# Optimization experiments

Measured on AMD Instinct MI355X. Metric: run time of the kernel, lower is better.

The kernel has to match this reference:

```python
import jax, jax.numpy as jnp
import numpy as np

NUM_HEADS = 32
NUM_KV_HEADS = 8
HEAD_DIM = 128
HIDDEN = 4096
ROPE_THETA = 10000.0
SLIDING_WINDOW = 1024
NEG_INF = -1e9


def _make_sliding_window_mask(q_len, kv_len, window):
    # additive mask: 0 where attendable (causal AND within window), -inf otherwise
    i = jnp.arange(q_len)[:, None]
    j = jnp.arange(kv_len)[None, :]
    allowed = (j <= i) & (j > i - window)
    return jnp.where(allowed, 0.0, NEG_INF).astype(jnp.float32)[None, None]  # [1,1,q,kv]


def _rope_tables(seq_len, head_dim, theta):
    inv_freq = 1.0 / (theta ** (jnp.arange(0, head_dim, 2, dtype=jnp.float32) / head_dim))
    t = jnp.arange(seq_len, dtype=jnp.float32)
    freqs = jnp.einsum('i,j->ij', t, inv_freq)        # [S, D/2]
    emb = jnp.concatenate([freqs, freqs], axis=-1)     # [S, D]
    return jnp.cos(emb), jnp.sin(emb)


def _rotate_half(x):
    d = x.shape[-1] // 2
    return jnp.concatenate([-x[..., d:], x[..., :d]], axis=-1)


def setup_inputs() -> dict:
    key = jax.random.key(0)
    ks = jax.random.split(key, 5)
    B, S = 1, 2048
    sc = 0.02
    hidden_states = jax.random.normal(ks[0], (B, S, HIDDEN), dtype=jnp.float32)
    Wq = jax.random.normal(ks[1], (HIDDEN, NUM_HEADS * HEAD_DIM), dtype=jnp.float32) * sc
    Wk = jax.random.normal(ks[2], (HIDDEN, NUM_KV_HEADS * HEAD_DIM), dtype=jnp.float32) * sc
    Wv = jax.random.normal(ks[3], (HIDDEN, NUM_KV_HEADS * HEAD_DIM), dtype=jnp.float32) * sc
    Wo = jax.random.normal(ks[4], (NUM_HEADS * HEAD_DIM, HIDDEN), dtype=jnp.float32) * sc
    attention_mask = _make_sliding_window_mask(S, S, SLIDING_WINDOW)
    position_ids = jnp.arange(S, dtype=jnp.int64)[None, :]
    return {"hidden_states": hidden_states, "attention_mask": attention_mask,
            "position_ids": position_ids, "Wq": Wq, "Wk": Wk, "Wv": Wv, "Wo": Wo}


def reference(hidden_states, attention_mask, position_ids, Wq, Wk, Wv, Wo):
    B, S, _ = hidden_states.shape
    # projections
    q = (hidden_states @ Wq).reshape(B, S, NUM_HEADS, HEAD_DIM).transpose(0, 2, 1, 3)      # [B,H,S,D]
    k = (hidden_states @ Wk).reshape(B, S, NUM_KV_HEADS, HEAD_DIM).transpose(0, 2, 1, 3)   # [B,Hk,S,D]
    v = (hidden_states @ Wv).reshape(B, S, NUM_KV_HEADS, HEAD_DIM).transpose(0, 2, 1, 3)
    # RoPE
    cos_t, sin_t = _rope_tables(S, HEAD_DIM, ROPE_THETA)
    cos = cos_t[position_ids][:, None]  # [B,1,S,D]
    sin = sin_t[position_ids][:, None]
    q = q * cos + _rotate_half(q) * sin
    k = k * cos + _rotate_half(k) * sin
    # repeat_kv (GQA): [B,Hk,S,D] -> [B,H,S,D]
    n_rep = NUM_HEADS // NUM_KV_HEADS
    k = jnp.repeat(k, n_rep, axis=1)
    v = jnp.repeat(v, n_rep, axis=1)
    # attention
    scores = jnp.einsum('bhqd,bhkd->bhqk', q, k) / np.sqrt(HEAD_DIM)
    scores = scores + attention_mask
    probs = jax.nn.softmax(scores, axis=-1)
    out = jnp.einsum('bhqk,bhkd->bhqd', probs, v)
    out = out.transpose(0, 2, 1, 3).reshape(B, S, HIDDEN)
    return out @ Wo
```

## Files before the change

kernel.cpp:

```cpp
#include <hip/hip_runtime.h>

typedef __attribute__((ext_vector_type(8))) short short8;
typedef __attribute__((ext_vector_type(4))) short s16x4;
typedef __attribute__((ext_vector_type(4))) float f32x4;
typedef unsigned short u16;
typedef unsigned int u32;

__device__ __forceinline__ u16 f2bf(float f) {
  union { float f; unsigned int u; } v; v.f = f;
  unsigned int r = (v.u + 0x7FFFu + ((v.u >> 16) & 1u)) >> 16;
  return (u16)r;
}
__device__ __forceinline__ float bf2f(u16 b) {
  union { unsigned int u; float f; } v; v.u = ((unsigned int)b) << 16;
  return v.f;
}
__device__ __forceinline__ void load_lds16(const void* g, void* l) {
  __builtin_amdgcn_global_load_lds((const __attribute__((address_space(1))) void*)g,
                                   (__attribute__((address_space(3))) void*)l, 16, 0, 0);
}

__global__ void cvt_f32_bf16_kernel(const float* __restrict__ in, u16* __restrict__ out, int n4) {
  int i = blockIdx.x * blockDim.x + threadIdx.x;
  if (i >= n4) return;
  float4 v = ((const float4*)in)[i];
  ushort4 o;
  o.x = f2bf(v.x); o.y = f2bf(v.y); o.z = f2bf(v.z); o.w = f2bf(v.w);
  ((ushort4*)out)[i] = o;
}

__global__ void combine_bf16_kernel(u16* __restrict__ d, const u16* __restrict__ p, int n8) {
  int i = blockIdx.x * blockDim.x + threadIdx.x;
  if (i >= n8) return;
  short8 a = ((const short8*)d)[i];
  short8 b = ((const short8*)p)[i];
  short8 o;
#pragma unroll
  for (int j = 0; j < 8; ++j) o[j] = (short)f2bf(bf2f((u16)a[j]) + bf2f((u16)b[j]));
  ((short8*)d)[i] = o;
}
__global__ void combine2_f32_kernel(float* __restrict__ out, const u16* __restrict__ p0,
                                    const u16* __restrict__ p1, int n8) {
  int i = blockIdx.x * blockDim.x + threadIdx.x;
  if (i >= n8) return;
  short8 a = ((const short8*)p0)[i];
  short8 b = ((const short8*)p1)[i];
  float4 o0, o1;
  o0.x = bf2f((u16)a[0]) + bf2f((u16)b[0]);
  o0.y = bf2f((u16)a[1]) + bf2f((u16)b[1]);
  o0.z = bf2f((u16)a[2]) + bf2f((u16)b[2]);
  o0.w = bf2f((u16)a[3]) + bf2f((u16)b[3]);
  o1.x = bf2f((u16)a[4]) + bf2f((u16)b[4]);
  o1.y = bf2f((u16)a[5]) + bf2f((u16)b[5]);
  o1.z = bf2f((u16)a[6]) + bf2f((u16)b[6]);
  o1.w = bf2f((u16)a[7]) + bf2f((u16)b[7]);
  ((float4*)out)[i * 2]     = o0;
  ((float4*)out)[i * 2 + 1] = o1;
}

__device__ __forceinline__ void tconv64_tile(const float* __restrict__ W, u16* __restrict__ Wt,
                                             int K, int N, int nb, int kb, int tid) {
  __shared__ float tile[64][65];
  int tx = tid & 15, ty = tid >> 4;
  const float* src = W + (size_t)(kb + ty) * N + nb + tx * 4;
#pragma unroll
  for (int i = 0; i < 4; ++i) {
    float4 v = *(const float4*)(src + (size_t)i * 16 * N);
    tile[ty + i * 16][tx * 4 + 0] = v.x;
    tile[ty + i * 16][tx * 4 + 1] = v.y;
    tile[ty + i * 16][tx * 4 + 2] = v.z;
    tile[ty + i * 16][tx * 4 + 3] = v.w;
  }
  __syncthreads();
  u16* dst = Wt + (size_t)(nb + ty) * K + kb + tx * 4;
#pragma unroll
  for (int i = 0; i < 4; ++i) {
    s16x4 o;
#pragma unroll
    for (int j = 0; j < 4; ++j) o[j] = (short)f2bf(tile[tx * 4 + j][ty + i * 16]);
    *(s16x4*)(dst + (size_t)i * 16 * K) = o;
  }
}

__global__ void tconv3_kernel(const float* __restrict__ Wq, const float* __restrict__ Wk,
                              const float* __restrict__ Wv, u16* __restrict__ WqT,
                              u16* __restrict__ WkvT) {
  int id = blockIdx.x;
  if (id < 4096)      tconv64_tile(Wq, WqT, 4096, 4096, (id & 63) * 64, (id >> 6) * 64, threadIdx.x);
  else if (id < 5120) { int t = id - 4096; tconv64_tile(Wk, WkvT, 4096, 1024, (t & 15) * 64, (t >> 4) * 64, threadIdx.x); }
  else                { int t = id - 5120; tconv64_tile(Wv, WkvT + (size_t)1024 * 4096, 4096, 1024, (t & 15) * 64, (t >> 4) * 64, threadIdx.x); }
}

__global__ void tconv1_kernel(const float* __restrict__ W, u16* __restrict__ Wt) {
  int id = blockIdx.x;
  tconv64_tile(W, Wt, 4096, 4096, (id & 63) * 64, (id >> 6) * 64, threadIdx.x);
}

__global__ void rope_kernel(u16* __restrict__ Qb, u16* __restrict__ Kb) {
  int idx = blockIdx.x * blockDim.x + threadIdx.x;
  u16* X; int ld, hmask, hshift, id; float scale;
  if (idx < 4194304) { X = Qb; ld = 4096; hmask = 31; hshift = 5; id = idx;           scale = 0.12751781828987514f; }
  else               { X = Kb; ld = 1024; hmask = 7;  hshift = 3; id = idx - 4194304; scale = 1.0f; }
  int j = id & 63;
  int t = id >> 6;
  int hh = t & hmask;
  int s = t >> hshift;
  float invf = exp2f(-(float)j * (13.287712379549449f / 64.0f));
  float ang = (float)s * invf;
  float sn, cs;
  sincosf(ang, &sn, &cs);
  u16* p = X + (size_t)s * ld + hh * 128 + j;
  float a = bf2f(p[0]), b = bf2f(p[64]);
  p[0]  = f2bf((a * cs - b * sn) * scale);
  p[64] = f2bf((b * cs + a * sn) * scale);
}

__global__ __launch_bounds__(256, 2) void gemm_kv_kernel(
    const u16* __restrict__ A, const u16* __restrict__ B,
    u16* __restrict__ Kb, u16* __restrict__ Vt, int N, int K) {
  __shared__ u16 As[2][128 * 64];
  __shared__ u16 Bs[2][128 * 64];
  int tid = threadIdx.x, lane = tid & 63, w = tid >> 6;
  int wr = w >> 1, wc = w & 1;
  int g = lane >> 4, q = lane & 15;
  int nbx = gridDim.x;
  int flat = blockIdx.y * nbx + blockIdx.x;
  int cpx = (nbx * gridDim.y) >> 3;
  flat = (flat & 7) * cpx + (flat >> 3);
  int m0 = (flat / nbx) * 128, n0 = (flat % nbx) * 128;
  f32x4 acc[4][4];
#pragma unroll
  for (int i = 0; i < 4; ++i)
#pragma unroll
    for (int j = 0; j < 4; ++j) acc[i][j] = (f32x4){0.f, 0.f, 0.f, 0.f};
  int srow = tid >> 3;
  int scol = ((tid & 7) ^ (srow & 7)) << 3;
  const u16* ga = A + (size_t)(m0 + srow) * K + scol;
  const u16* gb = B + (size_t)(n0 + srow) * K + scol;
  int xorm = (q & 7) << 3;
  int arow = wr * 64 + q;
  int brow = wc * 64 + q;
  int nt = K >> 6;

  auto stage = [&](int buf, int t) {
    const u16* pa = ga + t * 64;
    const u16* pb = gb + t * 64;
#pragma unroll
    for (int it = 0; it < 4; ++it) {
      load_lds16(pa + (size_t)it * 32 * K, (char*)(&As[buf][0]) + (it * 256 + w * 64) * 16);
      load_lds16(pb + (size_t)it * 32 * K, (char*)(&Bs[buf][0]) + (it * 256 + w * 64) * 16);
    }
  };

  stage(0, 0);
  stage(1, 1);
  asm volatile("s_waitcnt vmcnt(8)" ::: "memory");
  __builtin_amdgcn_s_barrier();
  for (int t = 0; t < nt; ++t) {
    int cur = t & 1;
    short8 af[2][4], bfr[2][4];
#pragma unroll
    for (int kb = 0; kb < 2; ++kb) {
      int col = (kb * 32 + g * 8) ^ xorm;
#pragma unroll
      for (int m = 0; m < 4; ++m) af[kb][m]  = *(const short8*)&As[cur][(arow + m * 16) * 64 + col];
#pragma unroll
      for (int n = 0; n < 4; ++n) bfr[kb][n] = *(const short8*)&Bs[cur][(brow + n * 16) * 64 + col];
    }
    asm volatile("s_waitcnt lgkmcnt(0)" ::: "memory");
    __builtin_amdgcn_s_barrier();
    if (t + 2 < nt) stage(cur, t + 2);
    __builtin_amdgcn_sched_barrier(0);
    __builtin_amdgcn_s_setprio(1);
#pragma unroll
    for (int kb = 0; kb < 2; ++kb)
#pragma unroll
      for (int m = 0; m < 4; ++m)
#pragma unroll
        for (int n = 0; n < 4; ++n)
          acc[m][n] = __builtin_amdgcn_mfma_f32_16x16x32_bf16(af[kb][m], bfr[kb][n], acc[m][n], 0, 0, 0);
    __builtin_amdgcn_s_setprio(0);
    if (t + 2 < nt)      { asm volatile("s_waitcnt vmcnt(8)" ::: "memory"); }
    else if (t + 1 < nt) { asm volatile("s_waitcnt vmcnt(0)" ::: "memory"); }
    __builtin_amdgcn_s_barrier();
  }
  int crow = m0 + wr * 64 + g * 4;
  int ccol = n0 + wc * 64 + q;
  if (n0 < 1024) {
#pragma unroll
    for (int m = 0; m < 4; ++m)
#pragma unroll
      for (int n = 0; n < 4; ++n)
#pragma unroll
        for (int r = 0; r < 4; ++r)
          Kb[(size_t)(crow + m * 16 + r) * 1024 + ccol + n * 16] = f2bf(acc[m][n][r]);
  } else {
#pragma unroll
    for (int n = 0; n < 4; ++n) {
      int vcol = ccol + n * 16 - 1024;
#pragma unroll
      for (int m = 0; m < 4; ++m) {
        s16x4 o;
#pragma unroll
        for (int r = 0; r < 4; ++r) o[r] = (short)f2bf(acc[m][n][r]);
        *(s16x4*)(Vt + (size_t)vcol * 2048 + crow + m * 16) = o;
      }
    }
  }
}

__global__ __launch_bounds__(512, 1) void gemm256_kernel(
    const u16* __restrict__ A, const u16* __restrict__ B,
    u16* __restrict__ C0, u16* __restrict__ C1, int N, int K, int KH) {
  __shared__ u16 As[2][256 * 64];
  __shared__ u16 Bs[2][256 * 64];
  int tid = threadIdx.x, lane = tid & 63, wid = tid >> 6;
  int wr = wid >> 2, wc = wid & 3;
  int g = lane >> 4, q = lane & 15;
  int id = blockIdx.z * gridDim.x * gridDim.y + blockIdx.y * gridDim.x + blockIdx.x;
  int tot = gridDim.x * gridDim.y * gridDim.z;
  int swz = (id & 7) * (tot >> 3) + (id >> 3);
  int perh = gridDim.x * gridDim.y;
  int z = swz / perh, rem = swz % perh;
  int m0 = (rem / gridDim.x) * 256, n0 = (rem % gridDim.x) * 256;
  int k0 = z * KH;
  f32x4 acc[8][4];
#pragma unroll
  for (int i = 0; i < 8; ++i)
#pragma unroll
    for (int j = 0; j < 4; ++j) acc[i][j] = (f32x4){0.f, 0.f, 0.f, 0.f};
  int srow = tid >> 3;
  int scol = ((tid & 7) ^ (srow & 7)) << 3;
  const u16* ga = A + (size_t)(m0 + srow) * K + k0 + scol;
  const u16* gb = B + (size_t)(n0 + srow) * K + k0 + scol;
  int xorm = (q & 7) << 3;
  int arow = wr * 128 + q;
  int brow = wc * 64 + q;
  int nt = KH >> 6;

  auto stage = [&](int buf, int t) {
    const u16* pa = ga + t * 64;
    const u16* pb = gb + t * 64;
#pragma unroll
    for (int it = 0; it < 4; ++it) {
      load_lds16(pa + (size_t)it * 64 * K, (char*)(&As[buf][0]) + it * 8192 + tid * 16);
      load_lds16(pb + (size_t)it * 64 * K, (char*)(&Bs[buf][0]) + it * 8192 + tid * 16);
    }
  };

  stage(0, 0);
  stage(1, 1);
  asm volatile("s_waitcnt vmcnt(8)" ::: "memory");
  __builtin_amdgcn_s_barrier();
  for (int t = 0; t < nt; ++t) {
    int cur = t & 1;
    int col0 = (g * 8) ^ xorm;
    short8 a0[8], b0[4];
#pragma unroll
    for (int m = 0; m < 8; ++m) a0[m] = *(const short8*)&As[cur][(arow + m * 16) * 64 + col0];
#pragma unroll
    for (int n = 0; n < 4; ++n) b0[n] = *(const short8*)&Bs[cur][(brow + n * 16) * 64 + col0];
    __builtin_amdgcn_s_setprio(1);
#pragma unroll
    for (int m = 0; m < 8; ++m)
#pragma unroll
      for (int n = 0; n < 4; ++n)
        acc[m][n] = __builtin_amdgcn_mfma_f32_16x16x32_bf16(a0[m], b0[n], acc[m][n], 0, 0, 0);
    __builtin_amdgcn_s_setprio(0);
    int col1 = (32 + g * 8) ^ xorm;
    short8 a1[8], b1[4];
#pragma unroll
    for (int m = 0; m < 8; ++m) a1[m] = *(const short8*)&As[cur][(arow + m * 16) * 64 + col1];
#pragma unroll
    for (int n = 0; n < 4; ++n) b1[n] = *(const short8*)&Bs[cur][(brow + n * 16) * 64 + col1];
    asm volatile("s_waitcnt lgkmcnt(0)" ::: "memory");
    __builtin_amdgcn_s_barrier();
    if (t + 2 < nt) stage(cur, t + 2);
    __builtin_amdgcn_sched_barrier(0);
    __builtin_amdgcn_s_setprio(1);
#pragma unroll
    for (int m = 0; m < 8; ++m)
#pragma unroll
      for (int n = 0; n < 4; ++n)
        acc[m][n] = __builtin_amdgcn_mfma_f32_16x16x32_bf16(a1[m], b1[n], acc[m][n], 0, 0, 0);
    __builtin_amdgcn_s_setprio(0);
    if (t + 2 < nt)      { asm volatile("s_waitcnt vmcnt(8)" ::: "memory"); }
    else if (t + 1 < nt) { asm volatile("s_waitcnt vmcnt(0)" ::: "memory"); }
    __builtin_amdgcn_s_barrier();
  }
  int crow = m0 + wr * 128 + g * 4;
  int ccol = n0 + wc * 64 + q;
  u16* dst = z ? C1 : C0;
#pragma unroll
  for (int fm = 0; fm < 8; ++fm)
#pragma unroll
    for (int fn = 0; fn < 4; ++fn)
#pragma unroll
      for (int r = 0; r < 4; ++r)
        dst[(size_t)(crow + fm * 16 + r) * N + ccol + fn * 16] = f2bf(acc[fm][fn][r]);
}

__global__ __launch_bounds__(512, 4) void attn_kernel(
    const u16* __restrict__ Q, const u16* __restrict__ Kg,
    const u16* __restrict__ Vt, u16* __restrict__ O) {
  __shared__ u16 Ks[2][64 * 128];
  __shared__ u16 Vs[2][128 * 64];
  int tid = threadIdx.x, lane = tid & 63, w = tid >> 6;
  int wg = w >> 2;
  int g = lane >> 4, q = lane & 15;
  int q0 = blockIdx.x * 128;
  int h = blockIdx.y, hk = h >> 2;
  int qbase = q0 + wg * 64;
  int qrow = qbase + (w & 3) * 16;
  int xorm = (lane & 7) << 3;
  short8 qf[4];
  {
    const u16* qp = Q + (size_t)(qrow + q) * 4096 + h * 128 + g * 8;
#pragma unroll
    for (int kk = 0; kk < 4; ++kk) qf[kk] = *(const short8*)(qp + kk * 32);
  }
  float mrow = -1e30f, lsum = 0.f;
  f32x4 of[8];
#pragma unroll
  for (int d = 0; d < 8; ++d) of[d] = (f32x4){0.f, 0.f, 0.f, 0.f};
  int bjt_lo = (q0 >= 1024) ? ((q0 - 1023) >> 6) : 0;
  int bjt_hi = (q0 + 64) >> 6;
  int wjt_lo = (qbase >= 1024) ? ((qbase - 1023) >> 6) : 0;
  int wjt_hi = qbase >> 6;
  int krow = tid >> 4;
  int kchunk = (tid & 15) ^ (krow & 7);
  const u16* kbase = Kg + (size_t)krow * 1024 + hk * 128 + (kchunk << 3);
  int vrow = tid >> 3;
  int vchunk = (tid & 7) ^ (vrow & 7);
  const u16* vbase = Vt + (size_t)(hk * 128 + vrow) * 2048 + (vchunk << 3);

  auto stageK = [&](int buf, int j0) {
    const u16* gp = kbase + (size_t)j0 * 1024;
#pragma unroll
    for (int it = 0; it < 2; ++it)
      load_lds16(gp + (size_t)it * 32 * 1024, (char*)(&Ks[buf][0]) + it * 8192 + tid * 16);
  };
  auto stageV = [&](int buf, int j0) {
    const u16* gp = vbase + j0;
#pragma unroll
    for (int it = 0; it < 2; ++it)
      load_lds16(gp + (size_t)it * 64 * 2048, (char*)(&Vs[buf][0]) + it * 8192 + tid * 16);
  };

  int cur = 0;
  stageK(0, bjt_lo << 6);
  stageV(0, bjt_lo << 6);
  asm volatile("s_waitcnt vmcnt(0)" ::: "memory");
  __syncthreads();
  for (int jt = bjt_lo; jt <= bjt_hi; ++jt) {
    int j0 = jt << 6;
    if (jt < bjt_hi) { stageK(cur ^ 1, j0 + 64); stageV(cur ^ 1, j0 + 64); }
    if (jt >= wjt_lo && jt <= wjt_hi) {
      f32x4 sf[4];
#pragma unroll
      for (int nt = 0; nt < 4; ++nt) sf[nt] = (f32x4){0.f, 0.f, 0.f, 0.f};
      const u16* ks = &Ks[cur][0];
      __builtin_amdgcn_s_setprio(1);
#pragma unroll
      for (int kk = 0; kk < 4; ++kk) {
        short8 qv = qf[kk];
        int col = (kk * 32 + g * 8) ^ xorm;
#pragma unroll
        for (int nt = 0; nt < 4; ++nt) {
          short8 kf = *(const short8*)&ks[(nt * 16 + q) * 128 + col];
          sf[nt] = __builtin_amdgcn_mfma_f32_16x16x32_bf16(kf, qv, sf[nt], 0, 0, 0);
        }
      }
      __builtin_amdgcn_s_setprio(0);
      float p[4][4];
#pragma unroll
      for (int nt = 0; nt < 4; ++nt)
#pragma unroll
        for (int r = 0; r < 4; ++r) p[nt][r] = sf[nt][r];
      if (j0 + 63 > qrow || j0 + 1009 <= qrow) {
        int qq = qrow + q;
        int kb = j0 + g * 4;
#pragma unroll
        for (int nt = 0; nt < 4; ++nt)
#pragma unroll
          for (int r = 0; r < 4; ++r) {
            int key = kb + nt * 16 + r;
            if (key > qq || key + 1024 <= qq) p[nt][r] = -1e9f;
          }
      }
      float tm = p[0][0];
#pragma unroll
      for (int nt = 0; nt < 4; ++nt)
#pragma unroll
        for (int r = 0; r < 4; ++r) tm = fmaxf(tm, p[nt][r]);
      tm = fmaxf(tm, __shfl_xor(tm, 16));
      tm = fmaxf(tm, __shfl_xor(tm, 32));
      if (__any(tm > mrow + 8.f)) {
        float nm = fmaxf(mrow, tm);
        float sc = __builtin_amdgcn_exp2f(mrow - nm);
        mrow = nm;
        lsum *= sc;
#pragma unroll
        for (int d = 0; d < 8; ++d) of[d] *= sc;
      }
      float ps = 0.f;
#pragma unroll
      for (int nt = 0; nt < 4; ++nt)
#pragma unroll
        for (int r = 0; r < 4; ++r) {
          float e = __builtin_amdgcn_exp2f(p[nt][r] - mrow);
          p[nt][r] = e;
          ps += e;
        }
      ps += __shfl_xor(ps, 16);
      ps += __shfl_xor(ps, 32);
      lsum += ps;
      u32 pk[4][2];
#pragma unroll
      for (int nt = 0; nt < 4; ++nt) {
        pk[nt][0] = __builtin_amdgcn_perm(__float_as_uint(p[nt][1]), __float_as_uint(p[nt][0]), 0x07060302u);
        pk[nt][1] = __builtin_amdgcn_perm(__float_as_uint(p[nt][3]), __float_as_uint(p[nt][2]), 0x07060302u);
      }
      int s0 = q + ((g & 1) ? 32 : 0);
      int s1 = s0 + 16;
      bool hi_sel = g >= 2;
      const u16* vs = &Vs[cur][0];
      __builtin_amdgcn_s_setprio(1);
#pragma unroll
      for (int kh = 0; kh < 2; ++kh) {
        int lo = kh * 2, hi = lo + 1;
        u32 a0 = (u32)__shfl((int)pk[lo][0], s0);
        u32 a1 = (u32)__shfl((int)pk[lo][1], s0);
        u32 b0 = (u32)__shfl((int)pk[hi][0], s0);
        u32 b1 = (u32)__shfl((int)pk[hi][1], s0);
        u32 a2 = (u32)__shfl((int)pk[lo][0], s1);
        u32 a3 = (u32)__shfl((int)pk[lo][1], s1);
        u32 b2 = (u32)__shfl((int)pk[hi][0], s1);
        u32 b3 = (u32)__shfl((int)pk[hi][1], s1);
        union { u32 u[4]; short8 s; } pb;
        pb.u[0] = hi_sel ? b0 : a0;
        pb.u[1] = hi_sel ? b1 : a1;
        pb.u[2] = hi_sel ? b2 : a2;
        pb.u[3] = hi_sel ? b3 : a3;
        int col = (kh * 32 + g * 8) ^ xorm;
#pragma unroll
        for (int dt = 0; dt < 8; ++dt) {
          short8 vv = *(const short8*)&vs[(dt * 16 + q) * 64 + col];
          of[dt] = __builtin_amdgcn_mfma_f32_16x16x32_bf16(vv, pb.s, of[dt], 0, 0, 0);
        }
      }
      __builtin_amdgcn_s_setprio(0);
    }
    asm volatile("s_waitcnt vmcnt(0)" ::: "memory");
    __builtin_amdgcn_s_barrier();
    cur ^= 1;
  }
  float inv = 1.f / lsum;
  u16* op = O + (size_t)(qrow + q) * 4096 + h * 128 + g * 4;
#pragma unroll
  for (int dt = 0; dt < 8; ++dt) {
    s16x4 o4;
#pragma unroll
    for (int r = 0; r < 4; ++r) o4[r] = (short)f2bf(of[dt][r] * inv);
    *(s16x4*)(op + dt * 16) = o4;
  }
}

extern "C" void kernel_launch(void* const* d_in, const int* in_sizes, int n_in,
                              void* d_out, int out_size, void* d_ws, size_t ws_size,
                              hipStream_t stream) {
  (void)in_sizes; (void)n_in; (void)out_size;
  const float* hs = (const float*)d_in[0];
  const float* Wq = (const float*)d_in[3];
  const float* Wk = (const float*)d_in[4];
  const float* Wv = (const float*)d_in[5];
  const float* Wo = (const float*)d_in[6];
  float* out = (float*)d_out;
  char* ws = (char*)d_ws;

  u16* Xb   = (u16*)(ws + 0);
  u16* Wt   = (u16*)(ws + 16777216);
  u16* WkvT = (u16*)(ws + 50331648);
  u16* Qb   = (u16*)(ws + 67108864);
  u16* Kb   = (u16*)(ws + 83886080);
  u16* Vtb  = (u16*)(ws + 88080384);
  u16* Ab   = (u16*)(ws + 96468992);
  u16* P1q  = Ab;
  u16* P0o  = WkvT;
  u16* P1o  = Qb;
  if (ws_size < 113246208u) return;

  cvt_f32_bf16_kernel<<<dim3(2097152 / 256), 256, 0, stream>>>(hs, Xb, 2097152);

  tconv3_kernel<<<dim3(6144), 256, 0, stream>>>(Wq, Wk, Wv, Wt, WkvT);

  gemm256_kernel<<<dim3(16, 8, 2), 512, 0, stream>>>(Xb, Wt, Qb, P1q, 4096, 4096, 2048);
  combine_bf16_kernel<<<dim3(4096), 256, 0, stream>>>(Qb, P1q, 1048576);

  gemm_kv_kernel<<<dim3(16, 16), 256, 0, stream>>>(Xb, WkvT, Kb, Vtb, 2048, 4096);

  rope_kernel<<<dim3(20480), 256, 0, stream>>>(Qb, Kb);

  attn_kernel<<<dim3(16, 32), 512, 0, stream>>>(Qb, Kb, Vtb, Ab);

  tconv1_kernel<<<dim3(4096), 256, 0, stream>>>(Wo, Wt);
  gemm256_kernel<<<dim3(16, 8, 2), 512, 0, stream>>>(Ab, Wt, P0o, P1o, 4096, 4096, 2048);
  combine2_f32_kernel<<<dim3(4096), 256, 0, stream>>>(out, P0o, P1o, 1048576);
}
```

Measured before the change: 324.0 us.

## Split-K KV projection with 256 tiles and fold Q partial combine into RoPE

The KV projection GEMM moves from 128x128 tiles on 256 blocks to 256x256 tiles with a 4-way K split (256 blocks), writing bf16 partials into the freed Wt buffer. A new combine kernel sums those partials into K and transposed V. The separate Q split-K combine kernel is removed, and its addition now happens inside the RoPE kernel. This cuts one launch and one full pass over Q, and gives the KV GEMM better tile reuse, at the cost of extra partial-buffer traffic and bf16 rounding of each partial.

New measurement: 311.7 us. 3.8% less time.

```diff
diff --git a/kernel.cpp b/kernel.cpp
--- a/kernel.cpp
+++ b/kernel.cpp
@@ -29,16 +29,6 @@
   ((ushort4*)out)[i] = o;
 }
 
-__global__ void combine_bf16_kernel(u16* __restrict__ d, const u16* __restrict__ p, int n8) {
-  int i = blockIdx.x * blockDim.x + threadIdx.x;
-  if (i >= n8) return;
-  short8 a = ((const short8*)d)[i];
-  short8 b = ((const short8*)p)[i];
-  short8 o;
-#pragma unroll
-  for (int j = 0; j < 8; ++j) o[j] = (short)f2bf(bf2f((u16)a[j]) + bf2f((u16)b[j]));
-  ((short8*)d)[i] = o;
-}
 __global__ void combine2_f32_kernel(float* __restrict__ out, const u16* __restrict__ p0,
                                     const u16* __restrict__ p1, int n8) {
   int i = blockIdx.x * blockDim.x + threadIdx.x;
@@ -58,6 +48,25 @@
   ((float4*)out)[i * 2 + 1] = o1;
 }
 
+__global__ void combine_kv_kernel(const u16* __restrict__ PKV, u16* __restrict__ Kb,
+                                  u16* __restrict__ Vt) {
+  int i = blockIdx.x * blockDim.x + threadIdx.x;
+  const u16* src; u16* dst; size_t off;
+  if (i < 262144) { off = (size_t)i; dst = Kb; src = PKV; }
+  else            { off = (size_t)(i - 262144); dst = Vt; src = PKV + 2097152; }
+  float s[8] = {0.f, 0.f, 0.f, 0.f, 0.f, 0.f, 0.f, 0.f};
+#pragma unroll
+  for (int z = 0; z < 4; ++z) {
+    short8 v = *(const short8*)(src + (size_t)z * 4194304 + off * 8);
+#pragma unroll
+    for (int j = 0; j < 8; ++j) s[j] += bf2f((u16)v[j]);
+  }
+  short8 o;
+#pragma unroll
+  for (int j = 0; j < 8; ++j) o[j] = (short)f2bf(s[j]);
+  ((short8*)dst)[off] = o;
+}
+
 __device__ __forceinline__ void tconv64_tile(const float* __restrict__ W, u16* __restrict__ Wt,
                                              int K, int N, int nb, int kb, int tid) {
   __shared__ float tile[64][65];
@@ -96,116 +105,34 @@
   tconv64_tile(W, Wt, 4096, 4096, (id & 63) * 64, (id >> 6) * 64, threadIdx.x);
 }
 
-__global__ void rope_kernel(u16* __restrict__ Qb, u16* __restrict__ Kb) {
+__global__ void rope_kernel(u16* __restrict__ Qb, const u16* __restrict__ Qp1, u16* __restrict__ Kb) {
   int idx = blockIdx.x * blockDim.x + threadIdx.x;
-  u16* X; int ld, hmask, hshift, id; float scale;
-  if (idx < 4194304) { X = Qb; ld = 4096; hmask = 31; hshift = 5; id = idx;           scale = 0.12751781828987514f; }
-  else               { X = Kb; ld = 1024; hmask = 7;  hshift = 3; id = idx - 4194304; scale = 1.0f; }
-  int j = id & 63;
-  int t = id >> 6;
-  int hh = t & hmask;
-  int s = t >> hshift;
-  float invf = exp2f(-(float)j * (13.287712379549449f / 64.0f));
-  float ang = (float)s * invf;
-  float sn, cs;
-  sincosf(ang, &sn, &cs);
-  u16* p = X + (size_t)s * ld + hh * 128 + j;
-  float a = bf2f(p[0]), b = bf2f(p[64]);
-  p[0]  = f2bf((a * cs - b * sn) * scale);
-  p[64] = f2bf((b * cs + a * sn) * scale);
-}
-
-__global__ __launch_bounds__(256, 2) void gemm_kv_kernel(
-    const u16* __restrict__ A, const u16* __restrict__ B,
-    u16* __restrict__ Kb, u16* __restrict__ Vt, int N, int K) {
-  __shared__ u16 As[2][128 * 64];
-  __shared__ u16 Bs[2][128 * 64];
-  int tid = threadIdx.x, lane = tid & 63, w = tid >> 6;
-  int wr = w >> 1, wc = w & 1;
-  int g = lane >> 4, q = lane & 15;
-  int nbx = gridDim.x;
-  int flat = blockIdx.y * nbx + blockIdx.x;
-  int cpx = (nbx * gridDim.y) >> 3;
-  flat = (flat & 7) * cpx + (flat >> 3);
-  int m0 = (flat / nbx) * 128, n0 = (flat % nbx) * 128;
-  f32x4 acc[4][4];
-#pragma unroll
-  for (int i = 0; i < 4; ++i)
-#pragma unroll
-    for (int j = 0; j < 4; ++j) acc[i][j] = (f32x4){0.f, 0.f, 0.f, 0.f};
-  int srow = tid >> 3;
-  int scol = ((tid & 7) ^ (srow & 7)) << 3;
-  const u16* ga = A + (size_t)(m0 + srow) * K + scol;
-  const u16* gb = B + (size_t)(n0 + srow) * K + scol;
-  int xorm = (q & 7) << 3;
-  int arow = wr * 64 + q;
-  int brow = wc * 64 + q;
-  int nt = K >> 6;
-
-  auto stage = [&](int buf, int t) {
-    const u16* pa = ga + t * 64;
-    const u16* pb = gb + t * 64;
-#pragma unroll
-    for (int it = 0; it < 4; ++it) {
-      load_lds16(pa + (size_t)it * 32 * K, (char*)(&As[buf][0]) + (it * 256 + w * 64) * 16);
-      load_lds16(pb + (size_t)it * 32 * K, (char*)(&Bs[buf][0]) + (it * 256 + w * 64) * 16);
-    }
-  };
-
-  stage(0, 0);
-  stage(1, 1);
-  asm volatile("s_waitcnt vmcnt(8)" ::: "memory");
-  __builtin_amdgcn_s_barrier();
-  for (int t = 0; t < nt; ++t) {
-    int cur = t & 1;
-    short8 af[2][4], bfr[2][4];
-#pragma unroll
-    for (int kb = 0; kb < 2; ++kb) {
-      int col = (kb * 32 + g * 8) ^ xorm;
-#pragma unroll
-      for (int m = 0; m < 4; ++m) af[kb][m]  = *(const short8*)&As[cur][(arow + m * 16) * 64 + col];
-#pragma unroll
-      for (int n = 0; n < 4; ++n) bfr[kb][n] = *(const short8*)&Bs[cur][(brow + n * 16) * 64 + col];
-    }
-    asm volatile("s_waitcnt lgkmcnt(0)" ::: "memory");
-    __builtin_amdgcn_s_barrier();
-    if (t + 2 < nt) stage(cur, t + 2);
-    __builtin_amdgcn_sched_barrier(0);
-    __builtin_amdgcn_s_setprio(1);
-#pragma unroll
-    for (int kb = 0; kb < 2; ++kb)
-#pragma unroll
-      for (int m = 0; m < 4; ++m)
-#pragma unroll
-        for (int n = 0; n < 4; ++n)
-          acc[m][n] = __builtin_amdgcn_mfma_f32_16x16x32_bf16(af[kb][m], bfr[kb][n], acc[m][n], 0, 0, 0);
-    __builtin_amdgcn_s_setprio(0);
-    if (t + 2 < nt)      { asm volatile("s_waitcnt vmcnt(8)" ::: "memory"); }
-    else if (t + 1 < nt) { asm volatile("s_waitcnt vmcnt(0)" ::: "memory"); }
-    __builtin_amdgcn_s_barrier();
-  }
-  int crow = m0 + wr * 64 + g * 4;
-  int ccol = n0 + wc * 64 + q;
-  if (n0 < 1024) {
-#pragma unroll
-    for (int m = 0; m < 4; ++m)
-#pragma unroll
-      for (int n = 0; n < 4; ++n)
-#pragma unroll
-        for (int r = 0; r < 4; ++r)
-          Kb[(size_t)(crow + m * 16 + r) * 1024 + ccol + n * 16] = f2bf(acc[m][n][r]);
+  int j, t, hh, s;
+  if (idx < 4194304) {
+    j = idx & 63; t = idx >> 6; hh = t & 31; s = t >> 5;
+    float invf = exp2f(-(float)j * (13.287712379549449f / 64.0f));
+    float ang = (float)s * invf;
+    float sn, cs;
+    sincosf(ang, &sn, &cs);
+    size_t base = (size_t)s * 4096 + hh * 128 + j;
+    u16* p = Qb + base;
+    const u16* p1 = Qp1 + base;
+    float a = bf2f(p[0]) + bf2f(p1[0]);
+    float b = bf2f(p[64]) + bf2f(p1[64]);
+    const float scale = 0.12751781828987514f;
+    p[0]  = f2bf((a * cs - b * sn) * scale);
+    p[64] = f2bf((b * cs + a * sn) * scale);
   } else {
-#pragma unroll
-    for (int n = 0; n < 4; ++n) {
-      int vcol = ccol + n * 16 - 1024;
-#pragma unroll
-      for (int m = 0; m < 4; ++m) {
-        s16x4 o;
-#pragma unroll
-        for (int r = 0; r < 4; ++r) o[r] = (short)f2bf(acc[m][n][r]);
-        *(s16x4*)(Vt + (size_t)vcol * 2048 + crow + m * 16) = o;
-      }
-    }
+    int id = idx - 4194304;
+    j = id & 63; t = id >> 6; hh = t & 7; s = t >> 3;
+    float invf = exp2f(-(float)j * (13.287712379549449f / 64.0f));
+    float ang = (float)s * invf;
+    float sn, cs;
+    sincosf(ang, &sn, &cs);
+    u16* p = Kb + (size_t)s * 1024 + hh * 128 + j;
+    float a = bf2f(p[0]), b = bf2f(p[64]);
+    p[0]  = f2bf(a * cs - b * sn);
+    p[64] = f2bf(b * cs + a * sn);
   }
 }
 
@@ -300,6 +227,110 @@
         dst[(size_t)(crow + fm * 16 + r) * N + ccol + fn * 16] = f2bf(acc[fm][fn][r]);
 }
 
+__global__ __launch_bounds__(512, 1) void gemm_kv256_kernel(
+    const u16* __restrict__ A, const u16* __restrict__ B,
+    u16* __restrict__ PKV, int K, int KH) {
+  __shared__ u16 As[2][256 * 64];
+  __shared__ u16 Bs[2][256 * 64];
+  int tid = threadIdx.x, lane = tid & 63, wid = tid >> 6;
+  int wr = wid >> 2, wc = wid & 3;
+  int g = lane >> 4, q = lane & 15;
+  int id = blockIdx.z * 64 + blockIdx.y * 8 + blockIdx.x;
+  int swz = (id & 7) * 32 + (id >> 3);
+  int z = swz >> 6, rem = swz & 63;
+  int m0 = (rem >> 3) * 256, n0 = (rem & 7) * 256;
+  int k0 = z * KH;
+  f32x4 acc[8][4];
+#pragma unroll
+  for (int i = 0; i < 8; ++i)
+#pragma unroll
+    for (int j = 0; j < 4; ++j) acc[i][j] = (f32x4){0.f, 0.f, 0.f, 0.f};
+  int srow = tid >> 3;
+  int scol = ((tid & 7) ^ (srow & 7)) << 3;
+  const u16* ga = A + (size_t)(m0 + srow) * K + k0 + scol;
+  const u16* gb = B + (size_t)(n0 + srow) * K + k0 + scol;
+  int xorm = (q & 7) << 3;
+  int arow = wr * 128 + q;
+  int brow = wc * 64 + q;
+  int nt = KH >> 6;
+
+  auto stage = [&](int buf, int t) {
+    const u16* pa = ga + t * 64;
+    const u16* pb = gb + t * 64;
+#pragma unroll
+    for (int it = 0; it < 4; ++it) {
+      load_lds16(pa + (size_t)it * 64 * K, (char*)(&As[buf][0]) + it * 8192 + tid * 16);
+      load_lds16(pb + (size_t)it * 64 * K, (char*)(&Bs[buf][0]) + it * 8192 + tid * 16);
+    }
+  };
+
+  stage(0, 0);
+  stage(1, 1);
+  asm volatile("s_waitcnt vmcnt(8)" ::: "memory");
+  __builtin_amdgcn_s_barrier();
+  for (int t = 0; t < nt; ++t) {
+    int cur = t & 1;
+    int col0 = (g * 8) ^ xorm;
+    short8 a0[8], b0[4];
+#pragma unroll
+    for (int m = 0; m < 8; ++m) a0[m] = *(const short8*)&As[cur][(arow + m * 16) * 64 + col0];
+#pragma unroll
+    for (int n = 0; n < 4; ++n) b0[n] = *(const short8*)&Bs[cur][(brow + n * 16) * 64 + col0];
+    __builtin_amdgcn_s_setprio(1);
+#pragma unroll
+    for (int m = 0; m < 8; ++m)
+#pragma unroll
+      for (int n = 0; n < 4; ++n)
+        acc[m][n] = __builtin_amdgcn_mfma_f32_16x16x32_bf16(a0[m], b0[n], acc[m][n], 0, 0, 0);
+    __builtin_amdgcn_s_setprio(0);
+    int col1 = (32 + g * 8) ^ xorm;
+    short8 a1[8], b1[4];
+#pragma unroll
+    for (int m = 0; m < 8; ++m) a1[m] = *(const short8*)&As[cur][(arow + m * 16) * 64 + col1];
+#pragma unroll
+    for (int n = 0; n < 4; ++n) b1[n] = *(const short8*)&Bs[cur][(brow + n * 16) * 64 + col1];
+    asm volatile("s_waitcnt lgkmcnt(0)" ::: "memory");
+    __builtin_amdgcn_s_barrier();
+    if (t + 2 < nt) stage(cur, t + 2);
+    __builtin_amdgcn_sched_barrier(0);
+    __builtin_amdgcn_s_setprio(1);
+#pragma unroll
+    for (int m = 0; m < 8; ++m)
+#pragma unroll
+      for (int n = 0; n < 4; ++n)
+        acc[m][n] = __builtin_amdgcn_mfma_f32_16x16x32_bf16(a1[m], b1[n], acc[m][n], 0, 0, 0);
+    __builtin_amdgcn_s_setprio(0);
+    if (t + 2 < nt)      { asm volatile("s_waitcnt vmcnt(8)" ::: "memory"); }
+    else if (t + 1 < nt) { asm volatile("s_waitcnt vmcnt(0)" ::: "memory"); }
+    __builtin_amdgcn_s_barrier();
+  }
+  int crow = m0 + wr * 128 + g * 4;
+  int ccol = n0 + wc * 64 + q;
+  u16* Kpart = PKV + (size_t)z * 4194304;
+  u16* Vpart = Kpart + 2097152;
+  if (n0 < 1024) {
+#pragma unroll
+    for (int fm = 0; fm < 8; ++fm)
+#pragma unroll
+      for (int fn = 0; fn < 4; ++fn)
+#pragma unroll
+        for (int r = 0; r < 4; ++r)
+          Kpart[(size_t)(crow + fm * 16 + r) * 1024 + ccol + fn * 16] = f2bf(acc[fm][fn][r]);
+  } else {
+#pragma unroll
+    for (int fn = 0; fn < 4; ++fn) {
+      int vcol = ccol + fn * 16 - 1024;
+#pragma unroll
+      for (int fm = 0; fm < 8; ++fm) {
+        s16x4 o;
+#pragma unroll
+        for (int r = 0; r < 4; ++r) o[r] = (short)f2bf(acc[fm][fn][r]);
+        *(s16x4*)(Vpart + (size_t)vcol * 2048 + crow + fm * 16) = o;
+      }
+    }
+  }
+}
+
 __global__ __launch_bounds__(512, 4) void attn_kernel(
     const u16* __restrict__ Q, const u16* __restrict__ Kg,
     const u16* __restrict__ Vt, u16* __restrict__ O) {
@@ -486,6 +517,7 @@
   u16* Vtb  = (u16*)(ws + 88080384);
   u16* Ab   = (u16*)(ws + 96468992);
   u16* P1q  = Ab;
+  u16* PKV  = Wt;
   u16* P0o  = WkvT;
   u16* P1o  = Qb;
   if (ws_size < 113246208u) return;
@@ -495,11 +527,11 @@
   tconv3_kernel<<<dim3(6144), 256, 0, stream>>>(Wq, Wk, Wv, Wt, WkvT);
 
   gemm256_kernel<<<dim3(16, 8, 2), 512, 0, stream>>>(Xb, Wt, Qb, P1q, 4096, 4096, 2048);
-  combine_bf16_kernel<<<dim3(4096), 256, 0, stream>>>(Qb, P1q, 1048576);
-
-  gemm_kv_kernel<<<dim3(16, 16), 256, 0, stream>>>(Xb, WkvT, Kb, Vtb, 2048, 4096);
-
-  rope_kernel<<<dim3(20480), 256, 0, stream>>>(Qb, Kb);
+
+  gemm_kv256_kernel<<<dim3(8, 8, 4), 512, 0, stream>>>(Xb, WkvT, PKV, 4096, 1024);
+  combine_kv_kernel<<<dim3(2048), 256, 0, stream>>>(PKV, Kb, Vtb);
+
+  rope_kernel<<<dim3(20480), 256, 0, stream>>>(Qb, P1q, Kb);
 
   attn_kernel<<<dim3(16, 32), 512, 0, stream>>>(Qb, Kb, Vtb, Ab);
 
```
